# Kernel optimization log

Hardware: AMD Instinct MI355X
Metric: run time of the kernel (lower is better)

The kernel has to match this reference:

```python
import jax, jax.numpy as jnp
import numpy as np

N_NODES = 50000
N_EDGES = 1600000
D_IN = 128
D_HID = 128


def setup_inputs() -> dict:
    key = jax.random.key(0)
    ks = jax.random.split(key, 6)
    edge_index = jax.random.randint(ks[0], (2, N_EDGES), 0, N_NODES, dtype=jnp.int32)
    emb = jax.random.normal(ks[1], (N_NODES, D_IN), dtype=jnp.float32) * 0.1
    W1 = jax.random.normal(ks[2], (D_IN, D_HID), dtype=jnp.float32) * (1.0 / np.sqrt(D_IN))
    b1 = jnp.zeros((D_HID,), dtype=jnp.float32)
    W2 = jax.random.normal(ks[3], (D_HID, D_HID), dtype=jnp.float32) * (1.0 / np.sqrt(D_HID))
    b2 = jnp.zeros((D_HID,), dtype=jnp.float32)
    head_w = jax.random.normal(ks[4], (D_HID, 1), dtype=jnp.float32) * (1.0 / np.sqrt(D_HID))
    head_b = jnp.zeros((1,), dtype=jnp.float32)
    return {"edge_index": edge_index, "emb": emb, "W1": W1, "b1": b1,
            "W2": W2, "b2": b2, "head_w": head_w, "head_b": head_b}


def _gcn_norm(edge_index, num_nodes):
    # PyG GCNConv default: add self-loops, sym-normalize D^-1/2 (A+I) D^-1/2.
    loops = jnp.arange(num_nodes, dtype=edge_index.dtype)
    src = jnp.concatenate([edge_index[0], loops])  # [E+N]
    dst = jnp.concatenate([edge_index[1], loops])  # [E+N]
    deg = jax.ops.segment_sum(jnp.ones_like(dst, dtype=jnp.float32), dst,
                              num_segments=num_nodes)  # [N], >=1 via self-loops
    dis = jax.lax.rsqrt(deg)
    norm = dis[src] * dis[dst]  # [E+N]
    return src, dst, norm


def _gcn_conv(x, W, b, src, dst, norm, num_nodes):
    h = x @ W                                  # [N, D] dense transform first
    msg = h[src] * norm[:, None]               # [E+N, D] gather + scale
    out = jax.ops.segment_sum(msg, dst, num_segments=num_nodes)  # scatter-add
    return out + b


def reference(edge_index, emb, W1, b1, W2, b2, head_w, head_b):
    src, dst, norm = _gcn_norm(edge_index, N_NODES)
    x = jax.nn.relu(_gcn_conv(emb, W1, b1, src, dst, norm, N_NODES))
    x = jax.nn.relu(_gcn_conv(x, W2, b2, src, dst, norm, N_NODES))
    scores = jax.nn.sigmoid(x @ head_w + head_b)[:, 0]  # [N]
    return scores
```

## Files before the change

### kernel.cpp

```cpp
#include <hip/hip_runtime.h>
#include <hip/hip_fp16.h>
#include <math.h>

#define D 128
#define D4 32
#define AP 136
#define AP8 144
#define NBUCK 256
#define EPB 8192
#define BCAP2 8192

typedef _Float16 f16x8 __attribute__((ext_vector_type(8)));
typedef float f32x4 __attribute__((ext_vector_type(4)));
typedef float f32x2 __attribute__((ext_vector_type(2)));


__global__ __launch_bounds__(256) void bucket_pass1(const int* __restrict__ src,
                                                    const int* __restrict__ dst,
                                                    int* __restrict__ bcnt,
                                                    unsigned* __restrict__ buckets,
                                                    int E, unsigned magicM) {
    __shared__ unsigned raw[EPB];
    __shared__ unsigned stage[EPB];
    __shared__ int lcnt[NBUCK], loff[NBUCK], gbase[NBUCK], sc[NBUCK];

    int t = threadIdx.x;
    int base = blockIdx.x * EPB;
    int nblk = min(EPB, E - base);
    lcnt[t] = 0;
    __syncthreads();

    for (int i = t; i < nblk; i += 256) {
        unsigned s = (unsigned)src[base + i];
        unsigned d = (unsigned)dst[base + i];
        unsigned pk = (s << 16) | d;
        raw[i] = pk;
        int b = (int)(((unsigned long long)d * magicM) >> 24);
        atomicAdd(&lcnt[b], 1);
    }
    __syncthreads();

    int v = lcnt[t];
    sc[t] = v;
    __syncthreads();
    for (int off = 1; off < 256; off <<= 1) {
        int x = (t >= off) ? sc[t - off] : 0;
        __syncthreads();
        sc[t] += x;
        __syncthreads();
    }
    loff[t] = sc[t] - v;
    gbase[t] = atomicAdd(&bcnt[t], v);
    lcnt[t] = 0;
    __syncthreads();

    for (int i = t; i < nblk; i += 256) {
        unsigned pk = raw[i];
        int b = (int)(((unsigned long long)(pk & 0xffffu) * magicM) >> 24);
        int p = atomicAdd(&lcnt[b], 1);
        stage[loff[b] + p] = pk;
    }
    __syncthreads();

    for (int i = t; i < nblk; i += 256) {
        unsigned pk = stage[i];
        int b = (int)(((unsigned long long)(pk & 0xffffu) * magicM) >> 24);
        int pos = gbase[b] + (i - loff[b]);
        if (pos < BCAP2) buckets[(size_t)b * BCAP2 + pos] = pk;
    }
}

__global__ void scan_bcnt_kernel(const int* __restrict__ bcnt, int* __restrict__ bstart,
                                 int* __restrict__ row_ptr, int N, int E) {
    __shared__ int sh[NBUCK];
    int t = threadIdx.x;
    int v = min(bcnt[t], BCAP2);
    sh[t] = v;
    __syncthreads();
    for (int off = 1; off < 256; off <<= 1) {
        int x = (t >= off) ? sh[t - off] : 0;
        __syncthreads();
        sh[t] += x;
        __syncthreads();
    }
    bstart[t] = sh[t] - v;
    if (t == 0) row_ptr[N] = E;
}

__global__ __launch_bounds__(256) void csr_pass2(const unsigned* __restrict__ buckets,
                                                 const int* __restrict__ bcnt,
                                                 const int* __restrict__ bstart,
                                                 int* __restrict__ row_ptr,
                                                 float* __restrict__ dis,
                                                 unsigned short* __restrict__ col,
                                                 int N, int npb) {
    __shared__ int cnt[256], sc[256], excl[256];
    __shared__ unsigned short estage[16384];

    int b = blockIdx.x;
    int t = threadIdx.x;
    int lo = b * npb;
    int nn = min(npb, N - lo);
    int n = min(bcnt[b], BCAP2);
    int base = bstart[b];
    const unsigned* bk = buckets + (size_t)b * BCAP2;

    cnt[t] = 0;
    __syncthreads();
    for (int i = t; i < n; i += 256) {
        int dl = (int)(bk[i] & 0xffffu) - lo;
        atomicAdd(&cnt[dl], 1);
    }
    __syncthreads();
    int v = cnt[t];
    sc[t] = v;
    __syncthreads();
    for (int off = 1; off < 256; off <<= 1) {
        int x = (t >= off) ? sc[t - off] : 0;
        __syncthreads();
        sc[t] += x;
        __syncthreads();
    }
    excl[t] = sc[t] - v;
    if (t < nn) {
        row_ptr[lo + t] = base + excl[t];
        dis[lo + t] = rsqrtf((float)v + 1.0f);
    }
    cnt[t] = 0;
    __syncthreads();
    for (int i = t; i < n; i += 256) {
        unsigned pk = bk[i];
        int dl = (int)(pk & 0xffffu) - lo;
        int p = atomicAdd(&cnt[dl], 1);
        estage[excl[dl] + p] = (unsigned short)(pk >> 16);
    }
    __syncthreads();
    for (int i = t; i < n; i += 256) col[base + i] = estage[i];
}


__global__ void prep_wt_kernel(const float* __restrict__ W, _Float16* __restrict__ Wt) {
    int i = blockIdx.x * 256 + threadIdx.x;
    int k = i >> 7, c = i & 127;
    Wt[c * 128 + k] = (_Float16)W[i];
}


#define GEMM_CORE                                                            \
    const uint4* Wt16 = (const uint4*)Wt;                                    \
    for (int i = t; i < 128 * 16; i += 256) {                                \
        int r = i >> 4, ch = i & 15;                                         \
        *(uint4*)&Ws[r * AP + ch * 8] = Wt16[i];                             \
    }                                                                        \
    __syncthreads();                                                         \
    int wave = t >> 6;                                                       \
    int lane = t & 63;                                                       \
    int m16 = lane & 15;                                                     \
    int quad = lane >> 4;                                                    \
    f32x4 acc[8];                                                            \
    for (int n = 0; n < 8; n++) acc[n] = (f32x4){0.f, 0.f, 0.f, 0.f};        \
    _Pragma("unroll")                                                        \
    for (int kc = 0; kc < 4; kc++) {                                         \
        f16x8 a = *(const f16x8*)&As[(wave * 16 + m16) * AP + kc * 32 + quad * 8]; \
        _Pragma("unroll")                                                    \
        for (int n = 0; n < 8; n++) {                                        \
            f16x8 bfrag = *(const f16x8*)&Ws[(n * 16 + m16) * AP + kc * 32 + quad * 8]; \
            acc[n] = __builtin_amdgcn_mfma_f32_16x16x32_f16(a, bfrag, acc[n], 0, 0, 0); \
        }                                                                    \
    }                                                                        \
    __syncthreads();                                                         \
    unsigned char* Cs8 = (unsigned char*)As;                                 \
    float dv[4];                                                             \
    _Pragma("unroll")                                                        \
    for (int r = 0; r < 4; r++) {                                            \
        int grow = row0 + wave * 16 + quad * 4 + r;                          \
        dv[r] = (grow < N) ? dis[grow] : 0.f;                                \
    }                                                                        \
    _Pragma("unroll")                                                        \
    for (int n = 0; n < 8; n++)                                              \
        _Pragma("unroll")                                                    \
        for (int r = 0; r < 4; r++) {                                        \
            float val = acc[n][r] * dv[r];                                   \
            int wq = __builtin_amdgcn_cvt_pk_fp8_f32(val, val, 0, false);    \
            Cs8[(wave * 16 + quad * 4 + r) * AP8 + n * 16 + m16] = (unsigned char)(wq & 0xff); \
        }                                                                    \
    __syncthreads();                                                         \
    uint4* C16 = (uint4*)C8;                                                 \
    for (int i = lane; i < 128; i += 64) {                                   \
        int r = i >> 3, ch = i & 7;                                          \
        int grow = row0 + wave * 16 + r;                                     \
        if (grow < N)                                                        \
            C16[(size_t)grow * 8 + ch] = *(const uint4*)&Cs8[(wave * 16 + r) * AP8 + ch * 16]; \
    }

__global__ __launch_bounds__(256) void gemm_f32a_fp8c(const float* __restrict__ A,
                                                      const _Float16* __restrict__ Wt,
                                                      const float* __restrict__ dis,
                                                      unsigned int* __restrict__ C8, int N) {
    __shared__ _Float16 As[64 * AP];
    __shared__ _Float16 Ws[128 * AP];
    int t = threadIdx.x;
    int row0 = blockIdx.x * 64;
    const float4* A4 = (const float4*)A;
    for (int i = t; i < 64 * 16; i += 256) {
        int r = i >> 4, ch = i & 15;
        uint4 v = make_uint4(0, 0, 0, 0);
        if (row0 + r < N) {
            float4 a0 = A4[(size_t)(row0 + r) * 32 + ch * 2];
            float4 a1 = A4[(size_t)(row0 + r) * 32 + ch * 2 + 1];
            __half2 h0 = __floats2half2_rn(a0.x, a0.y);
            __half2 h1 = __floats2half2_rn(a0.z, a0.w);
            __half2 h2 = __floats2half2_rn(a1.x, a1.y);
            __half2 h3 = __floats2half2_rn(a1.z, a1.w);
            v.x = *(unsigned*)&h0; v.y = *(unsigned*)&h1;
            v.z = *(unsigned*)&h2; v.w = *(unsigned*)&h3;
        }
        *(uint4*)&As[r * AP + ch * 8] = v;
    }
    GEMM_CORE
}

__global__ __launch_bounds__(256) void gemm_f16a_fp8c(const _Float16* __restrict__ A,
                                                      const _Float16* __restrict__ Wt,
                                                      const float* __restrict__ dis,
                                                      unsigned int* __restrict__ C8, int N) {
    __shared__ _Float16 As[64 * AP];
    __shared__ _Float16 Ws[128 * AP];
    int t = threadIdx.x;
    int row0 = blockIdx.x * 64;
    const uint4* A16 = (const uint4*)A;
    for (int i = t; i < 64 * 16; i += 256) {
        int r = i >> 4, ch = i & 15;
        uint4 v = make_uint4(0, 0, 0, 0);
        if (row0 + r < N) v = A16[(size_t)(row0 + r) * 16 + ch];
        *(uint4*)&As[r * AP + ch * 8] = v;
    }
    GEMM_CORE
}


__device__ __forceinline__ void acc8(float4& a, unsigned int u) {
    f32x2 lo = __builtin_amdgcn_cvt_pk_f32_fp8((int)u, false);
    f32x2 hi = __builtin_amdgcn_cvt_pk_f32_fp8((int)u, true);
    a.x += lo[0]; a.y += lo[1]; a.z += hi[0]; a.w += hi[1];
}

#define AGG8_BODY                                                               \
    float4 acc = make_float4(0.f, 0.f, 0.f, 0.f);                               \
    acc8(acc, t8[(size_t)node * D4 + lane]);        \
    int e0 = row_ptr[node], e1 = row_ptr[node + 1];                             \
    int deg = e1 - e0;                                                          \
    for (int base = 0; base < deg; base += 32) {                                \
        int cnt = min(32, deg - base);                                          \
        int myc = (base + lane < deg) ? (int)col[e0 + base + lane] : 0;         \
        int j = 0;                                                              \
        for (; j + 8 <= cnt; j += 8) {                                          \
            int s0 = __shfl(myc, j + 0, 32); int s1 = __shfl(myc, j + 1, 32);   \
            int s2 = __shfl(myc, j + 2, 32); int s3 = __shfl(myc, j + 3, 32);   \
            int s4 = __shfl(myc, j + 4, 32); int s5 = __shfl(myc, j + 5, 32);   \
            int s6 = __shfl(myc, j + 6, 32); int s7 = __shfl(myc, j + 7, 32);   \
            unsigned int u0 = t8[(size_t)s0 * D4 + lane];                       \
            unsigned int u1 = t8[(size_t)s1 * D4 + lane];                       \
            unsigned int u2 = t8[(size_t)s2 * D4 + lane];                       \
            unsigned int u3 = t8[(size_t)s3 * D4 + lane];                       \
            unsigned int u4 = t8[(size_t)s4 * D4 + lane];                       \
            unsigned int u5 = t8[(size_t)s5 * D4 + lane];                       \
            unsigned int u6 = t8[(size_t)s6 * D4 + lane];                       \
            unsigned int u7 = t8[(size_t)s7 * D4 + lane];                       \
            acc8(acc, u0); acc8(acc, u1); acc8(acc, u2); acc8(acc, u3);         \
            acc8(acc, u4); acc8(acc, u5); acc8(acc, u6); acc8(acc, u7);         \
        }                                                                       \
        for (; j < cnt; j++) {                                                  \
            int s = __shfl(myc, j, 32);                                         \
            acc8(acc, t8[(size_t)s * D4 + lane]);                               \
        }                                                                       \
    }                                                                           \
    float di = dis[node];                                                       \
    float4 bb = ((const float4*)bias)[lane];                                    \
    float4 o;                                                                   \
    o.x = fmaxf(fmaf(di, acc.x, bb.x), 0.f);                                    \
    o.y = fmaxf(fmaf(di, acc.y, bb.y), 0.f);                                    \
    o.z = fmaxf(fmaf(di, acc.z, bb.z), 0.f);                                    \
    o.w = fmaxf(fmaf(di, acc.w, bb.w), 0.f);

__global__ void agg_fp8_kernel(const unsigned int* __restrict__ t8, const float* __restrict__ bias,
                               const int* __restrict__ row_ptr, const unsigned short* __restrict__ col,
                               const float* __restrict__ dis, _Float16* __restrict__ xout, int N) {
    int t = threadIdx.x;
    int node = blockIdx.x * 8 + (t >> 5);
    int lane = t & 31;
    if (node >= N) return;
    AGG8_BODY
    __half2 q0 = __floats2half2_rn(o.x, o.y);
    __half2 q1 = __floats2half2_rn(o.z, o.w);
    uint2 u;
    u.x = *(unsigned int*)&q0;
    u.y = *(unsigned int*)&q1;
    ((uint2*)xout)[(size_t)node * D4 + lane] = u;
}

__global__ void agg_head_fp8_kernel(const unsigned int* __restrict__ t8, const float* __restrict__ bias,
                                    const int* __restrict__ row_ptr, const unsigned short* __restrict__ col,
                                    const float* __restrict__ dis,
                                    const float* __restrict__ head_w, const float* __restrict__ head_b,
                                    float* __restrict__ out, int N) {
    int t = threadIdx.x;
    int node = blockIdx.x * 8 + (t >> 5);
    int lane = t & 31;
    if (node >= N) return;
    AGG8_BODY
    float4 wv = ((const float4*)head_w)[lane];
    float s = o.x * wv.x + o.y * wv.y + o.z * wv.z + o.w * wv.w;
    for (int m = 1; m < 32; m <<= 1) s += __shfl_xor(s, m, 64);
    if (lane == 0) {
        float v = s + head_b[0];
        out[node] = 1.0f / (1.0f + expf(-v));
    }
}


extern "C" void kernel_launch(void* const* d_in, const int* in_sizes, int n_in,
                              void* d_out, int out_size, void* d_ws, size_t ws_size,
                              hipStream_t stream) {
    const int*   edge   = (const int*)d_in[0];
    const float* emb    = (const float*)d_in[1];
    const float* W1     = (const float*)d_in[2];
    const float* b1     = (const float*)d_in[3];
    const float* W2     = (const float*)d_in[4];
    const float* b2     = (const float*)d_in[5];
    const float* head_w = (const float*)d_in[6];
    const float* head_b = (const float*)d_in[7];
    float* out = (float*)d_out;

    int E = in_sizes[0] / 2;
    int N = in_sizes[1] / D;
    const int* srcp = edge;
    const int* dstp = edge + E;

    char* w = (char*)d_ws;
    auto alloc = [&](size_t bytes) -> char* {
        char* p = w;
        w += (bytes + 15) & ~(size_t)15;
        return p;
    };
    unsigned int*   t8      = (unsigned int*)alloc((size_t)N * D);
    _Float16*       x1h     = (_Float16*)alloc((size_t)N * D * 2);
    unsigned*       buckets = (unsigned*)alloc((size_t)NBUCK * BCAP2 * 4);
    _Float16*       Wt1     = (_Float16*)alloc((size_t)D * D * 2);
    _Float16*       Wt2     = (_Float16*)alloc((size_t)D * D * 2);
    unsigned short* col     = (unsigned short*)alloc((size_t)E * 2);
    int*            bcnt    = (int*)alloc(NBUCK * 4);
    int*            bstart  = (int*)alloc(NBUCK * 4);
    int*            row_ptr = (int*)alloc((size_t)(N + 1) * 4);
    float*          dis     = (float*)alloc((size_t)N * 4);

    int npb = (N + NBUCK - 1) / NBUCK;
    unsigned magicM = (16777216u + (unsigned)npb - 1) / (unsigned)npb;
    int gP1 = (E + EPB - 1) / EPB;
    int gG = (N + 63) / 64;
    int gA = (N + 7) / 8;

    (void)hipMemsetAsync(bcnt, 0, NBUCK * 4, stream);

    prep_wt_kernel<<<64, 256, 0, stream>>>(W1, Wt1);
    prep_wt_kernel<<<64, 256, 0, stream>>>(W2, Wt2);

    bucket_pass1<<<gP1, 256, 0, stream>>>(srcp, dstp, bcnt, buckets, E, magicM);
    scan_bcnt_kernel<<<1, 256, 0, stream>>>(bcnt, bstart, row_ptr, N, E);
    csr_pass2<<<NBUCK, 256, 0, stream>>>(buckets, bcnt, bstart, row_ptr, dis, col, N, npb);

    gemm_f32a_fp8c<<<gG, 256, 0, stream>>>(emb, Wt1, dis, t8, N);
    agg_fp8_kernel<<<gA, 256, 0, stream>>>(t8, b1, row_ptr, col, dis, x1h, N);
    gemm_f16a_fp8c<<<gG, 256, 0, stream>>>(x1h, Wt2, dis, t8, N);
    agg_head_fp8_kernel<<<gA, 256, 0, stream>>>(t8, b2, row_ptr, col, dis,
                                                head_w, head_b, out, N);
}
```

Baseline: 211.7 us.

## Merge prep kernels and memset, fold bucket scan into CSR pass, unroll full-chunk gather

Folds the two weight-transpose launches and the bucket-counter memset into one prep kernel. It also removes the separate single-block scan kernel by having every csr_pass2 block redo the 256-entry prefix scan itself. Together these cut launch count and serial gaps between kernels. In the aggregation, full 32-neighbour chunks now issue all 32 gathers before accumulating, which exposes more memory-level parallelism at the cost of more registers per thread.

```diff
diff --git a/kernel.cpp b/kernel.cpp
--- a/kernel.cpp
+++ b/kernel.cpp
@@ -13,6 +13,20 @@
 typedef _Float16 f16x8 __attribute__((ext_vector_type(8)));
 typedef float f32x4 __attribute__((ext_vector_type(4)));
 typedef float f32x2 __attribute__((ext_vector_type(2)));
+
+
+__global__ void prep_all_kernel(const float* __restrict__ W1, _Float16* __restrict__ Wt1,
+                                const float* __restrict__ W2, _Float16* __restrict__ Wt2,
+                                int* __restrict__ bcnt) {
+    int t = threadIdx.x;
+    if (blockIdx.x == 0) bcnt[t] = 0;
+    int half = blockIdx.x & 63;
+    const float* W = (blockIdx.x < 64) ? W1 : W2;
+    _Float16* Wt   = (blockIdx.x < 64) ? Wt1 : Wt2;
+    int i = half * 256 + t;
+    int k = i >> 7, c = i & 127;
+    Wt[c * 128 + k] = (_Float16)W[i];
+}
 
 
 __global__ __launch_bounds__(256) void bucket_pass1(const int* __restrict__ src,
@@ -70,39 +84,34 @@
     }
 }
 
-__global__ void scan_bcnt_kernel(const int* __restrict__ bcnt, int* __restrict__ bstart,
-                                 int* __restrict__ row_ptr, int N, int E) {
-    __shared__ int sh[NBUCK];
-    int t = threadIdx.x;
-    int v = min(bcnt[t], BCAP2);
-    sh[t] = v;
-    __syncthreads();
-    for (int off = 1; off < 256; off <<= 1) {
-        int x = (t >= off) ? sh[t - off] : 0;
-        __syncthreads();
-        sh[t] += x;
-        __syncthreads();
-    }
-    bstart[t] = sh[t] - v;
-    if (t == 0) row_ptr[N] = E;
-}
-
 __global__ __launch_bounds__(256) void csr_pass2(const unsigned* __restrict__ buckets,
                                                  const int* __restrict__ bcnt,
-                                                 const int* __restrict__ bstart,
                                                  int* __restrict__ row_ptr,
                                                  float* __restrict__ dis,
                                                  unsigned short* __restrict__ col,
-                                                 int N, int npb) {
+                                                 int N, int npb, int E) {
     __shared__ int cnt[256], sc[256], excl[256];
     __shared__ unsigned short estage[16384];
 
     int b = blockIdx.x;
     int t = threadIdx.x;
+
+    int bv = min(bcnt[t], BCAP2);
+    sc[t] = bv;
+    __syncthreads();
+    for (int off = 1; off < 256; off <<= 1) {
+        int x = (t >= off) ? sc[t - off] : 0;
+        __syncthreads();
+        sc[t] += x;
+        __syncthreads();
+    }
+    int base = sc[b] - min(bcnt[b], BCAP2);
+    if (b == 0 && t == 0) row_ptr[N] = E;
+    __syncthreads();
+
     int lo = b * npb;
     int nn = min(npb, N - lo);
     int n = min(bcnt[b], BCAP2);
-    int base = bstart[b];
     const unsigned* bk = buckets + (size_t)b * BCAP2;
 
     cnt[t] = 0;
@@ -136,13 +145,6 @@
     }
     __syncthreads();
     for (int i = t; i < n; i += 256) col[base + i] = estage[i];
-}
-
-
-__global__ void prep_wt_kernel(const float* __restrict__ W, _Float16* __restrict__ Wt) {
-    int i = blockIdx.x * 256 + threadIdx.x;
-    int k = i >> 7, c = i & 127;
-    Wt[c * 128 + k] = (_Float16)W[i];
 }
 
 
@@ -253,26 +255,37 @@
     for (int base = 0; base < deg; base += 32) {                                \
         int cnt = min(32, deg - base);                                          \
         int myc = (base + lane < deg) ? (int)col[e0 + base + lane] : 0;         \
-        int j = 0;                                                              \
-        for (; j + 8 <= cnt; j += 8) {                                          \
-            int s0 = __shfl(myc, j + 0, 32); int s1 = __shfl(myc, j + 1, 32);   \
-            int s2 = __shfl(myc, j + 2, 32); int s3 = __shfl(myc, j + 3, 32);   \
-            int s4 = __shfl(myc, j + 4, 32); int s5 = __shfl(myc, j + 5, 32);   \
-            int s6 = __shfl(myc, j + 6, 32); int s7 = __shfl(myc, j + 7, 32);   \
-            unsigned int u0 = t8[(size_t)s0 * D4 + lane];                       \
-            unsigned int u1 = t8[(size_t)s1 * D4 + lane];                       \
-            unsigned int u2 = t8[(size_t)s2 * D4 + lane];                       \
-            unsigned int u3 = t8[(size_t)s3 * D4 + lane];                       \
-            unsigned int u4 = t8[(size_t)s4 * D4 + lane];                       \
-            unsigned int u5 = t8[(size_t)s5 * D4 + lane];                       \
-            unsigned int u6 = t8[(size_t)s6 * D4 + lane];                       \
-            unsigned int u7 = t8[(size_t)s7 * D4 + lane];                       \
-            acc8(acc, u0); acc8(acc, u1); acc8(acc, u2); acc8(acc, u3);         \
-            acc8(acc, u4); acc8(acc, u5); acc8(acc, u6); acc8(acc, u7);         \
-        }                                                                       \
-        for (; j < cnt; j++) {                                                  \
-            int s = __shfl(myc, j, 32);                                         \
-            acc8(acc, t8[(size_t)s * D4 + lane]);                               \
+        if (cnt == 32) {                                                        \
+            unsigned u[32];                                                     \
+            _Pragma("unroll")                                                   \
+            for (int j = 0; j < 32; j++) {                                      \
+                int s = __shfl(myc, j, 32);                                     \
+                u[j] = t8[(size_t)s * D4 + lane];                               \
+            }                                                                   \
+            _Pragma("unroll")                                                   \
+            for (int j = 0; j < 32; j++) acc8(acc, u[j]);                       \
+        } else {                                                                \
+            int j = 0;                                                          \
+            for (; j + 8 <= cnt; j += 8) {                                      \
+                int s0 = __shfl(myc, j + 0, 32); int s1 = __shfl(myc, j + 1, 32); \
+                int s2 = __shfl(myc, j + 2, 32); int s3 = __shfl(myc, j + 3, 32); \
+                int s4 = __shfl(myc, j + 4, 32); int s5 = __shfl(myc, j + 5, 32); \
+                int s6 = __shfl(myc, j + 6, 32); int s7 = __shfl(myc, j + 7, 32); \
+                unsigned int u0 = t8[(size_t)s0 * D4 + lane];                   \
+                unsigned int u1 = t8[(size_t)s1 * D4 + lane];                   \
+                unsigned int u2 = t8[(size_t)s2 * D4 + lane];                   \
+                unsigned int u3 = t8[(size_t)s3 * D4 + lane];                   \
+                unsigned int u4 = t8[(size_t)s4 * D4 + lane];                   \
+                unsigned int u5 = t8[(size_t)s5 * D4 + lane];                   \
+                unsigned int u6 = t8[(size_t)s6 * D4 + lane];                   \
+                unsigned int u7 = t8[(size_t)s7 * D4 + lane];                   \
+                acc8(acc, u0); acc8(acc, u1); acc8(acc, u2); acc8(acc, u3);     \
+                acc8(acc, u4); acc8(acc, u5); acc8(acc, u6); acc8(acc, u7);     \
+            }                                                                   \
+            for (; j < cnt; j++) {                                              \
+                int s = __shfl(myc, j, 32);                                     \
+                acc8(acc, t8[(size_t)s * D4 + lane]);                           \
+            }                                                                   \
         }                                                                       \
     }                                                                           \
     float di = dis[node];                                                       \
@@ -350,7 +363,6 @@
     _Float16*       Wt2     = (_Float16*)alloc((size_t)D * D * 2);
     unsigned short* col     = (unsigned short*)alloc((size_t)E * 2);
     int*            bcnt    = (int*)alloc(NBUCK * 4);
-    int*            bstart  = (int*)alloc(NBUCK * 4);
     int*            row_ptr = (int*)alloc((size_t)(N + 1) * 4);
     float*          dis     = (float*)alloc((size_t)N * 4);
 
@@ -360,14 +372,9 @@
     int gG = (N + 63) / 64;
     int gA = (N + 7) / 8;
 
-    (void)hipMemsetAsync(bcnt, 0, NBUCK * 4, stream);
-
-    prep_wt_kernel<<<64, 256, 0, stream>>>(W1, Wt1);
-    prep_wt_kernel<<<64, 256, 0, stream>>>(W2, Wt2);
-
+    prep_all_kernel<<<128, 256, 0, stream>>>(W1, Wt1, W2, Wt2, bcnt);
     bucket_pass1<<<gP1, 256, 0, stream>>>(srcp, dstp, bcnt, buckets, E, magicM);
-    scan_bcnt_kernel<<<1, 256, 0, stream>>>(bcnt, bstart, row_ptr, N, E);
-    csr_pass2<<<NBUCK, 256, 0, stream>>>(buckets, bcnt, bstart, row_ptr, dis, col, N, npb);
+    csr_pass2<<<NBUCK, 256, 0, stream>>>(buckets, bcnt, row_ptr, dis, col, N, npb, E);
 
     gemm_f32a_fp8c<<<gG, 256, 0, stream>>>(emb, Wt1, dis, t8, N);
     agg_fp8_kernel<<<gA, 256, 0, stream>>>(t8, b1, row_ptr, col, dis, x1h, N);
```

New measurement: 215.7 us. Within noise of the previous version (+1.9%).
